# Kernel tuning notes

Measured on AMD Instinct MI355X. Metric: run time of the kernel, lower is better.

## Reference

```python
import jax, jax.numpy as jnp
import numpy as np

E = 8      # num_experts
D = 512    # input feature dim
H1 = 512   # expert_hidden[0]
H2 = 256   # expert_hidden[1]
Y = 256    # y_dim
B = 8192   # batch
ALPHA = 0.2


def setup_inputs() -> dict:
    key = jax.random.key(0)
    ks = jax.random.split(key, 8)
    h = jax.random.normal(ks[0], (B, D), dtype=jnp.float32)
    gate_id = jax.random.randint(ks[1], (B,), 0, E, dtype=jnp.int64)
    # Per-expert MLP parameters, stacked over expert axis (Glorot-ish scale)
    W1 = jax.random.normal(ks[2], (E, D, H1), dtype=jnp.float32) * (1.0 / np.sqrt(D))
    b1 = jnp.zeros((E, H1), dtype=jnp.float32)
    W2 = jax.random.normal(ks[3], (E, H1, H2), dtype=jnp.float32) * (1.0 / np.sqrt(H1))
    b2 = jnp.zeros((E, H2), dtype=jnp.float32)
    W3 = jax.random.normal(ks[4], (E, H2, Y), dtype=jnp.float32) * (1.0 / np.sqrt(H2))
    b3 = jnp.zeros((E, Y), dtype=jnp.float32)
    return {"h": h, "gate_id": gate_id, "W1": W1, "b1": b1,
            "W2": W2, "b2": b2, "W3": W3, "b3": b3}


def _leaky(x):
    return jnp.where(x > 0, x, ALPHA * x)


def reference(h, gate_id, W1, b1, W2, b2, W3, b3):
    # Hard routing: gate_id = clip(round(gate_id), 0, E-1)
    g = jnp.clip(jnp.round(gate_id.astype(jnp.float32)).astype(jnp.int32), 0, E - 1)
    # Dense all-experts compute (jit-friendly, no dynamic shapes), then select
    # the routed expert's output per row. Same math as dispatch/stitch.
    a1 = _leaky(jnp.einsum('bd,edh->ebh', h, W1) + b1[:, None, :])   # [E,B,H1]
    a2 = _leaky(jnp.einsum('ebh,ehk->ebk', a1, W2) + b2[:, None, :]) # [E,B,H2]
    y = jnp.einsum('ebk,eky->eby', a2, W3) + b3[:, None, :]          # [E,B,Y]
    out = y[g, jnp.arange(h.shape[0])]                                # [B,Y]
    return out
```

## Files before the change

kernel.cpp:

```cpp
#include <hip/hip_runtime.h>
#include <stdint.h>

#define NE 8
#define ND 512
#define NH1 512
#define NH2 256
#define NY 256
#define NB 8192
#define BM3 48
#define NBPE 24
#define NBLK (NE * NBPE)
#define W1T64 (NE * (ND/64) * (NH1/64))
#define W2T64 (NE * (NH1/64) * (NH2/64))
#define W3T64 (NE * (NH2/64) * (NY/64))
#define WTT64 (W1T64 + W2T64 + W3T64)

typedef float f32x4 __attribute__((ext_vector_type(4)));
typedef __bf16 bf16x8 __attribute__((ext_vector_type(8)));
typedef unsigned short u16x8 __attribute__((ext_vector_type(8)));

__device__ __forceinline__ unsigned short f2bf(float f) {
  unsigned int u = __float_as_uint(f);
  u += 0x7fffu + ((u >> 16) & 1u);
  return (unsigned short)(u >> 16);
}

__device__ __forceinline__ int clampe(int g) {
  return g < 0 ? 0 : (g > NE - 1 ? NE - 1 : g);
}



__global__ __launch_bounds__(256)
void prep_k(const int* __restrict__ gate,
            const float* __restrict__ W1, const float* __restrict__ W2,
            const float* __restrict__ W3,
            unsigned short* __restrict__ w1f, unsigned short* __restrict__ w2f,
            unsigned short* __restrict__ w3f,
            int* __restrict__ meta, int* __restrict__ perm)
{
  __shared__ char sm[17024] __attribute__((aligned(16)));
  int b = blockIdx.x, t = threadIdx.x;

  if (b < WTT64) {
    float* ldsf = (float*)sm;
    const float* src; unsigned short* dst; int K, N, idx;
    if (b < W1T64)          { src = W1; dst = w1f; K = ND;  N = NH1; idx = b; }
    else if (b < W1T64 + W2T64) { src = W2; dst = w2f; K = NH1; N = NH2; idx = b - W1T64; }
    else                    { src = W3; dst = w3f; K = NH2; N = NY;  idx = b - W1T64 - W2T64; }
    int ntn = N >> 6, ntk = K >> 6;
    int n0 = (idx % ntn) * 64;
    int k0 = ((idx / ntn) % ntk) * 64;
    int g  = idx / (ntn * ntk);

    {
      int r  = t >> 2;
      int c4 = t & 3;
      const float* s = src + (size_t)g * K * N + (size_t)(k0 + r) * N + n0;
      #pragma unroll
      for (int i = 0; i < 4; i++) {
        float4 v = *(const float4*)(s + (i * 4 + c4) * 4);
        *(float4*)(ldsf + r * 65 + (i * 4 + c4) * 4) = v;
      }
    }
    __syncthreads();

    unsigned short* d = dst + (size_t)g * K * N;
    #pragma unroll
    for (int ii = 0; ii < 2; ii++) {
      int idx2 = ii * 256 + t;
      int lane = idx2 & 63;
      int f    = (idx2 >> 6) & 3;
      int kt   = idx2 >> 8;
      int kl   = kt * 32 + (lane >> 4) * 8;
      int nl   = f * 16 + (lane & 15);
      union { u16x8 v; unsigned short u[8]; } pk;
      #pragma unroll
      for (int j = 0; j < 8; j++)
        pk.u[j] = f2bf(ldsf[(kl + j) * 65 + nl]);
      int ktg = (k0 >> 5) + kt;
      int fg  = (n0 >> 4) + f;
      *(u16x8*)(d + (((size_t)ktg * (N >> 4) + fg) * 64 + lane) * 8) = pk.v;
    }
    return;
  }

  unsigned int* lcnt_lo = (unsigned int*)sm;
  unsigned int* lcnt_hi = lcnt_lo + 256;
  int* pre   = (int*)(sm + 2048);
  int* cnt8  = (int*)(sm + 2048 + 8192);
  int* offs8 = cnt8 + 8;

  unsigned int gp[8];
  unsigned int clo = 0, chi = 0;
  #pragma unroll
  for (int i = 0; i < 32; i++) {
    int g = clampe(gate[t * 32 + i]);
    if ((i & 3) == 0) gp[i >> 2] = 0;
    gp[i >> 2] |= (unsigned int)g << (8 * (i & 3));
    if (g < 4) clo += 1u << (8 * g);
    else       chi += 1u << (8 * (g - 4));
  }
  lcnt_lo[t] = clo;
  lcnt_hi[t] = chi;
  __syncthreads();

  int wave = t >> 6, lane = t & 63;
  #pragma unroll
  for (int pass = 0; pass < 2; pass++) {
    int e = wave + pass * 4;
    int carry = 0;
    #pragma unroll
    for (int ch = 0; ch < 4; ch++) {
      int idx = ch * 64 + lane;
      unsigned int word = (e < 4) ? lcnt_lo[idx] : lcnt_hi[idx];
      int v = (int)((word >> (8 * (e & 3))) & 255u);
      int s = v;
      #pragma unroll
      for (int d = 1; d < 64; d <<= 1) {
        int up = __shfl_up(s, d, 64);
        if (lane >= d) s += up;
      }
      pre[e * 256 + idx] = carry + s - v;
      carry += __shfl(s, 63, 64);
    }
    if (lane == 0) cnt8[e] = carry;
  }
  __syncthreads();

  if (t == 0) {
    int off = 0;
    for (int e = 0; e < NE; e++) {
      int cc = cnt8[e];
      meta[e] = cc;
      meta[8 + e] = off;
      offs8[e] = off;
      meta[16 + e] = (cc + BM3 - 1) / BM3;
      meta[32 + e] = 0;
      off += cc;
    }
  }
  __syncthreads();

  unsigned int rlo = 0, rhi = 0;
  #pragma unroll
  for (int i = 0; i < 32; i++) {
    int g = (int)((gp[i >> 2] >> (8 * (i & 3))) & 255u);
    int r;
    if (g < 4) { r = (int)((rlo >> (8 * g)) & 255u);       rlo += 1u << (8 * g); }
    else       { r = (int)((rhi >> (8 * (g - 4))) & 255u); rhi += 1u << (8 * (g - 4)); }
    perm[offs8[g] + pre[g * 256 + t] + r] = t * 32 + i;
  }
}

__global__ __launch_bounds__(512, 4)
void mlp_k(const float* __restrict__ h,
           const float* __restrict__ b1, const float* __restrict__ b2,
           const float* __restrict__ b3,
           float* __restrict__ out,
           int* __restrict__ meta, const int* __restrict__ perm,
           const unsigned short* __restrict__ w1f,
           const unsigned short* __restrict__ w2f,
           const unsigned short* __restrict__ w3f)
{
  __shared__ unsigned short sA[BM3 * 520];
  __shared__ unsigned short sB[BM3 * 520];
  __shared__ int permc[BM3];
  __shared__ int sclaim[2];

  int tid  = threadIdx.x;

  if (tid == 0) {
    int xcc = (int)__builtin_amdgcn_s_getreg((31 << 11) | 20) & (NE - 1);
    int ce = -1, cti = 0;
    for (int a = 0; a < NE; a++) {
      int ee = (xcc + a) & (NE - 1);
      int ntl = meta[16 + ee];
      if (ntl <= 0) continue;
      int tk = atomicAdd(&meta[32 + ee], 1);
      if (tk < ntl) { ce = ee; cti = tk; break; }
    }
    sclaim[0] = ce; sclaim[1] = cti;
  }
  __syncthreads();

  int e = sclaim[0];
  if (e < 0) return;
  int trow = sclaim[1];
  int cnt  = meta[e];
  int off  = meta[8 + e];
  int row0 = trow * BM3;

  if (tid < BM3) {
    int grow = row0 + tid;
    permc[tid] = (grow < cnt) ? perm[off + grow] : 0;
  }
  __syncthreads();

  int wave = tid >> 6, lane = tid & 63;
  int lm = lane & 15, quad = lane >> 4;

  {
    int rr0 = tid >> 4;
    int cb  = (tid & 15) * 8;
    for (int r = rr0; r < BM3; r += 32) {
      const float* hrow = h + (size_t)permc[r] * ND;
      #pragma unroll
      for (int jj = 0; jj < 4; jj++) {
        int col = cb + jj * 128;
        float4 f0 = *(const float4*)(hrow + col);
        float4 f1 = *(const float4*)(hrow + col + 4);
        union { u16x8 v; unsigned short u[8]; } pk;
        pk.u[0] = f2bf(f0.x); pk.u[1] = f2bf(f0.y); pk.u[2] = f2bf(f0.z); pk.u[3] = f2bf(f0.w);
        pk.u[4] = f2bf(f1.x); pk.u[5] = f2bf(f1.y); pk.u[6] = f2bf(f1.z); pk.u[7] = f2bf(f1.w);
        *(u16x8*)(sA + r * 520 + col) = pk.v;
      }
    }
  }
  __syncthreads();

  f32x4 zero = {0.f, 0.f, 0.f, 0.f};

  {
    f32x4 acc[3][4];
    #pragma unroll
    for (int mi = 0; mi < 3; mi++)
      #pragma unroll
      for (int ni = 0; ni < 4; ni++)
        acc[mi][ni] = zero;
    const unsigned short* Wb = w1f + (size_t)e * ND * NH1 + ((size_t)(wave * 4) * 64 + lane) * 8;
    bf16x8 cur[4], nxt[4];
    #pragma unroll
    for (int ni = 0; ni < 4; ni++)
      cur[ni] = *reinterpret_cast<const bf16x8*>(Wb + ni * 512);
    for (int t = 0; t < 16; t++) {
      int tn = (t + 1 < 16) ? t + 1 : t;
      #pragma unroll
      for (int ni = 0; ni < 4; ni++)
        nxt[ni] = *reinterpret_cast<const bf16x8*>(Wb + (size_t)tn * 16384 + ni * 512);
      bf16x8 af[3];
      #pragma unroll
      for (int mi = 0; mi < 3; mi++)
        af[mi] = *reinterpret_cast<const bf16x8*>(sA + (mi * 16 + lm) * 520 + t * 32 + quad * 8);
      #pragma unroll
      for (int mi = 0; mi < 3; mi++)
        #pragma unroll
        for (int ni = 0; ni < 4; ni++)
          acc[mi][ni] = __builtin_amdgcn_mfma_f32_16x16x32_bf16(af[mi], cur[ni], acc[mi][ni], 0, 0, 0);
      #pragma unroll
      for (int ni = 0; ni < 4; ni++)
        cur[ni] = nxt[ni];
    }
    #pragma unroll
    for (int mi = 0; mi < 3; mi++)
      #pragma unroll
      for (int ni = 0; ni < 4; ni++) {
        int col = (wave * 4 + ni) * 16 + lm;
        float bv = b1[e * NH1 + col];
        #pragma unroll
        for (int r = 0; r < 4; r++) {
          int row = mi * 16 + quad * 4 + r;
          float v = acc[mi][ni][r] + bv;
          v = (v > 0.f) ? v : 0.2f * v;
          sB[row * 520 + col] = f2bf(v);
        }
      }
  }
  __syncthreads();

  {
    f32x4 acc[3][2];
    #pragma unroll
    for (int mi = 0; mi < 3; mi++)
      #pragma unroll
      for (int ni = 0; ni < 2; ni++)
        acc[mi][ni] = zero;
    const unsigned short* Wb = w2f + (size_t)e * NH1 * NH2 + ((size_t)(wave * 2) * 64 + lane) * 8;
    bf16x8 cur[2], nxt[2];
    #pragma unroll
    for (int ni = 0; ni < 2; ni++)
      cur[ni] = *reinterpret_cast<const bf16x8*>(Wb + ni * 512);
    for (int t = 0; t < 16; t++) {
      int tn = (t + 1 < 16) ? t + 1 : t;
      #pragma unroll
      for (int ni = 0; ni < 2; ni++)
        nxt[ni] = *reinterpret_cast<const bf16x8*>(Wb + (size_t)tn * 8192 + ni * 512);
      bf16x8 af[3];
      #pragma unroll
      for (int mi = 0; mi < 3; mi++)
        af[mi] = *reinterpret_cast<const bf16x8*>(sB + (mi * 16 + lm) * 520 + t * 32 + quad * 8);
      #pragma unroll
      for (int mi = 0; mi < 3; mi++)
        #pragma unroll
        for (int ni = 0; ni < 2; ni++)
          acc[mi][ni] = __builtin_amdgcn_mfma_f32_16x16x32_bf16(af[mi], cur[ni], acc[mi][ni], 0, 0, 0);
      #pragma unroll
      for (int ni = 0; ni < 2; ni++)
        cur[ni] = nxt[ni];
    }
    #pragma unroll
    for (int mi = 0; mi < 3; mi++)
      #pragma unroll
      for (int ni = 0; ni < 2; ni++) {
        int col = (wave * 2 + ni) * 16 + lm;
        float bv = b2[e * NH2 + col];
        #pragma unroll
        for (int r = 0; r < 4; r++) {
          int row = mi * 16 + quad * 4 + r;
          float v = acc[mi][ni][r] + bv;
          v = (v > 0.f) ? v : 0.2f * v;
          sA[row * 264 + col] = f2bf(v);
        }
      }
  }
  __syncthreads();

  {
    f32x4 acc[3][2];
    #pragma unroll
    for (int mi = 0; mi < 3; mi++)
      #pragma unroll
      for (int ni = 0; ni < 2; ni++)
        acc[mi][ni] = zero;
    const unsigned short* Wb = w3f + (size_t)e * NH2 * NY + ((size_t)(wave * 2) * 64 + lane) * 8;
    bf16x8 cur[2], nxt[2];
    #pragma unroll
    for (int ni = 0; ni < 2; ni++)
      cur[ni] = *reinterpret_cast<const bf16x8*>(Wb + ni * 512);
    for (int t = 0; t < 8; t++) {
      int tn = (t + 1 < 8) ? t + 1 : t;
      #pragma unroll
      for (int ni = 0; ni < 2; ni++)
        nxt[ni] = *reinterpret_cast<const bf16x8*>(Wb + (size_t)tn * 8192 + ni * 512);
      bf16x8 af[3];
      #pragma unroll
      for (int mi = 0; mi < 3; mi++)
        af[mi] = *reinterpret_cast<const bf16x8*>(sA + (mi * 16 + lm) * 264 + t * 32 + quad * 8);
      #pragma unroll
      for (int mi = 0; mi < 3; mi++)
        #pragma unroll
        for (int ni = 0; ni < 2; ni++)
          acc[mi][ni] = __builtin_amdgcn_mfma_f32_16x16x32_bf16(af[mi], cur[ni], acc[mi][ni], 0, 0, 0);
      #pragma unroll
      for (int ni = 0; ni < 2; ni++)
        cur[ni] = nxt[ni];
    }
    #pragma unroll
    for (int mi = 0; mi < 3; mi++)
      #pragma unroll
      for (int ni = 0; ni < 2; ni++) {
        int col = (wave * 2 + ni) * 16 + lm;
        float bv = b3[e * NY + col];
        #pragma unroll
        for (int r = 0; r < 4; r++) {
          int row = mi * 16 + quad * 4 + r;
          int grow = row0 + row;
          if (grow < cnt) {
            float v = acc[mi][ni][r] + bv;
            __builtin_nontemporal_store(v, &out[(size_t)permc[row] * NY + col]);
          }
        }
      }
  }
}

extern "C" void kernel_launch(void* const* d_in, const int* in_sizes, int n_in,
                              void* d_out, int out_size, void* d_ws, size_t ws_size,
                              hipStream_t stream) {
  (void)in_sizes; (void)n_in; (void)out_size; (void)ws_size;
  const float* h  = (const float*)d_in[0];
  const int* gate = (const int*)d_in[1];
  const float* W1 = (const float*)d_in[2];
  const float* b1 = (const float*)d_in[3];
  const float* W2 = (const float*)d_in[4];
  const float* b2 = (const float*)d_in[5];
  const float* W3 = (const float*)d_in[6];
  const float* b3 = (const float*)d_in[7];
  float* out = (float*)d_out;

  char* ws = (char*)d_ws;
  int* meta = (int*)ws;
  int* perm = (int*)(ws + 8192);
  unsigned short* w1f = (unsigned short*)(ws + 8192 + 32768);
  unsigned short* w2f = w1f + (size_t)NE * ND * NH1;
  unsigned short* w3f = w2f + (size_t)NE * NH1 * NH2;

  prep_k<<<WTT64 + 1, 256, 0, stream>>>(gate, W1, W2, W3, w1f, w2f, w3f, meta, perm);
  mlp_k<<<NBLK, 512, 0, stream>>>(h, b1, b2, b3, out, meta, perm, w1f, w2f, w3f);
}
```

Baseline: 113.8 us.

## Fuse weight prep and routed MLP into one cooperative kernel with grid sync

Merges the bf16 weight-conversion/routing-prep kernel and the expert MLP kernel into a single cooperative launch. Blocks first loop over the prep work units, then hit a grid-wide barrier, then compute their tile assignment statically from per-expert tile counts instead of claiming tiles with atomics. This removes one kernel launch and its inter-kernel gap. In exchange it adds grid-sync cost, the limits of a cooperative launch, and weaker XCC locality than the old atomic claim.

```diff
diff --git a/kernel.cpp b/kernel.cpp
--- a/kernel.cpp
+++ b/kernel.cpp
@@ -1,5 +1,8 @@
 #include <hip/hip_runtime.h>
+#include <hip/hip_cooperative_groups.h>
 #include <stdint.h>
+
+namespace cg = cooperative_groups;
 
 #define NE 8
 #define ND 512
@@ -8,12 +11,12 @@
 #define NY 256
 #define NB 8192
 #define BM3 48
-#define NBPE 24
-#define NBLK (NE * NBPE)
+#define NBLK 192
 #define W1T64 (NE * (ND/64) * (NH1/64))
 #define W2T64 (NE * (NH1/64) * (NH2/64))
 #define W3T64 (NE * (NH2/64) * (NY/64))
 #define WTT64 (W1T64 + W2T64 + W3T64)
+#define NUNIT (WTT64 + 1)
 
 typedef float f32x4 __attribute__((ext_vector_type(4)));
 typedef __bf16 bf16x8 __attribute__((ext_vector_type(8)));
@@ -30,163 +33,154 @@
 }
 
 
-
-__global__ __launch_bounds__(256)
-void prep_k(const int* __restrict__ gate,
-            const float* __restrict__ W1, const float* __restrict__ W2,
-            const float* __restrict__ W3,
-            unsigned short* __restrict__ w1f, unsigned short* __restrict__ w2f,
-            unsigned short* __restrict__ w3f,
-            int* __restrict__ meta, int* __restrict__ perm)
-{
-  __shared__ char sm[17024] __attribute__((aligned(16)));
-  int b = blockIdx.x, t = threadIdx.x;
-
-  if (b < WTT64) {
-    float* ldsf = (float*)sm;
-    const float* src; unsigned short* dst; int K, N, idx;
-    if (b < W1T64)          { src = W1; dst = w1f; K = ND;  N = NH1; idx = b; }
-    else if (b < W1T64 + W2T64) { src = W2; dst = w2f; K = NH1; N = NH2; idx = b - W1T64; }
-    else                    { src = W3; dst = w3f; K = NH2; N = NY;  idx = b - W1T64 - W2T64; }
-    int ntn = N >> 6, ntk = K >> 6;
-    int n0 = (idx % ntn) * 64;
-    int k0 = ((idx / ntn) % ntk) * 64;
-    int g  = idx / (ntn * ntk);
-
-    {
-      int r  = t >> 2;
-      int c4 = t & 3;
-      const float* s = src + (size_t)g * K * N + (size_t)(k0 + r) * N + n0;
-      #pragma unroll
-      for (int i = 0; i < 4; i++) {
-        float4 v = *(const float4*)(s + (i * 4 + c4) * 4);
-        *(float4*)(ldsf + r * 65 + (i * 4 + c4) * 4) = v;
-      }
-    }
-    __syncthreads();
-
-    unsigned short* d = dst + (size_t)g * K * N;
-    #pragma unroll
-    for (int ii = 0; ii < 2; ii++) {
-      int idx2 = ii * 256 + t;
-      int lane = idx2 & 63;
-      int f    = (idx2 >> 6) & 3;
-      int kt   = idx2 >> 8;
-      int kl   = kt * 32 + (lane >> 4) * 8;
-      int nl   = f * 16 + (lane & 15);
-      union { u16x8 v; unsigned short u[8]; } pk;
-      #pragma unroll
-      for (int j = 0; j < 8; j++)
-        pk.u[j] = f2bf(ldsf[(kl + j) * 65 + nl]);
-      int ktg = (k0 >> 5) + kt;
-      int fg  = (n0 >> 4) + f;
-      *(u16x8*)(d + (((size_t)ktg * (N >> 4) + fg) * 64 + lane) * 8) = pk.v;
-    }
-    return;
-  }
-
-  unsigned int* lcnt_lo = (unsigned int*)sm;
-  unsigned int* lcnt_hi = lcnt_lo + 256;
-  int* pre   = (int*)(sm + 2048);
-  int* cnt8  = (int*)(sm + 2048 + 8192);
-  int* offs8 = cnt8 + 8;
-
-  unsigned int gp[8];
-  unsigned int clo = 0, chi = 0;
-  #pragma unroll
-  for (int i = 0; i < 32; i++) {
-    int g = clampe(gate[t * 32 + i]);
-    if ((i & 3) == 0) gp[i >> 2] = 0;
-    gp[i >> 2] |= (unsigned int)g << (8 * (i & 3));
-    if (g < 4) clo += 1u << (8 * g);
-    else       chi += 1u << (8 * (g - 4));
-  }
-  lcnt_lo[t] = clo;
-  lcnt_hi[t] = chi;
-  __syncthreads();
-
-  int wave = t >> 6, lane = t & 63;
-  #pragma unroll
-  for (int pass = 0; pass < 2; pass++) {
-    int e = wave + pass * 4;
-    int carry = 0;
-    #pragma unroll
-    for (int ch = 0; ch < 4; ch++) {
-      int idx = ch * 64 + lane;
-      unsigned int word = (e < 4) ? lcnt_lo[idx] : lcnt_hi[idx];
-      int v = (int)((word >> (8 * (e & 3))) & 255u);
-      int s = v;
-      #pragma unroll
-      for (int d = 1; d < 64; d <<= 1) {
-        int up = __shfl_up(s, d, 64);
-        if (lane >= d) s += up;
-      }
-      pre[e * 256 + idx] = carry + s - v;
-      carry += __shfl(s, 63, 64);
-    }
-    if (lane == 0) cnt8[e] = carry;
-  }
-  __syncthreads();
-
-  if (t == 0) {
-    int off = 0;
-    for (int e = 0; e < NE; e++) {
-      int cc = cnt8[e];
-      meta[e] = cc;
-      meta[8 + e] = off;
-      offs8[e] = off;
-      meta[16 + e] = (cc + BM3 - 1) / BM3;
-      meta[32 + e] = 0;
-      off += cc;
-    }
-  }
-  __syncthreads();
-
-  unsigned int rlo = 0, rhi = 0;
-  #pragma unroll
-  for (int i = 0; i < 32; i++) {
-    int g = (int)((gp[i >> 2] >> (8 * (i & 3))) & 255u);
-    int r;
-    if (g < 4) { r = (int)((rlo >> (8 * g)) & 255u);       rlo += 1u << (8 * g); }
-    else       { r = (int)((rhi >> (8 * (g - 4))) & 255u); rhi += 1u << (8 * (g - 4)); }
-    perm[offs8[g] + pre[g * 256 + t] + r] = t * 32 + i;
-  }
-}
-
 __global__ __launch_bounds__(512, 4)
-void mlp_k(const float* __restrict__ h,
+void moe_k(const float* __restrict__ h, const int* __restrict__ gate,
+           const float* __restrict__ W1, const float* __restrict__ W2,
+           const float* __restrict__ W3,
            const float* __restrict__ b1, const float* __restrict__ b2,
            const float* __restrict__ b3,
            float* __restrict__ out,
-           int* __restrict__ meta, const int* __restrict__ perm,
-           const unsigned short* __restrict__ w1f,
-           const unsigned short* __restrict__ w2f,
-           const unsigned short* __restrict__ w3f)
+           int* __restrict__ meta, int* __restrict__ perm,
+           unsigned short* __restrict__ w1f, unsigned short* __restrict__ w2f,
+           unsigned short* __restrict__ w3f)
 {
-  __shared__ unsigned short sA[BM3 * 520];
-  __shared__ unsigned short sB[BM3 * 520];
-  __shared__ int permc[BM3];
-  __shared__ int sclaim[2];
-
-  int tid  = threadIdx.x;
-
-  if (tid == 0) {
-    int xcc = (int)__builtin_amdgcn_s_getreg((31 << 11) | 20) & (NE - 1);
-    int ce = -1, cti = 0;
-    for (int a = 0; a < NE; a++) {
-      int ee = (xcc + a) & (NE - 1);
+  __shared__ char smem[100032] __attribute__((aligned(16)));
+  unsigned short* sA = (unsigned short*)smem;
+  unsigned short* sB = sA + BM3 * 520;
+  int* permc = (int*)(smem + 99840);
+
+  int bid = blockIdx.x, tid = threadIdx.x;
+
+  for (int ui = 0; ui < 5; ui++) {
+    int u = bid + ui * NBLK;
+    if (u >= NUNIT) break;
+
+    if (u < WTT64) {
+      float* ldsf = (float*)smem;
+      const float* src; unsigned short* dst; int K, N, idx;
+      if (u < W1T64)              { src = W1; dst = w1f; K = ND;  N = NH1; idx = u; }
+      else if (u < W1T64 + W2T64) { src = W2; dst = w2f; K = NH1; N = NH2; idx = u - W1T64; }
+      else                        { src = W3; dst = w3f; K = NH2; N = NY;  idx = u - W1T64 - W2T64; }
+      int ntn = N >> 6, ntk = K >> 6;
+      int n0 = (idx % ntn) * 64;
+      int k0 = ((idx / ntn) % ntk) * 64;
+      int g  = idx / (ntn * ntk);
+
+      {
+        int r  = tid >> 3;
+        int c4 = tid & 7;
+        const float* s = src + (size_t)g * K * N + (size_t)(k0 + r) * N + n0;
+        #pragma unroll
+        for (int i = 0; i < 2; i++) {
+          float4 v = *(const float4*)(s + (i * 8 + c4) * 4);
+          *(float4*)(ldsf + r * 65 + (i * 8 + c4) * 4) = v;
+        }
+      }
+      __syncthreads();
+
+      {
+        unsigned short* d = dst + (size_t)g * K * N;
+        int lane = tid & 63;
+        int f    = (tid >> 6) & 3;
+        int kt   = tid >> 8;
+        int kl   = kt * 32 + (lane >> 4) * 8;
+        int nl   = f * 16 + (lane & 15);
+        union { u16x8 v; unsigned short u[8]; } pk;
+        #pragma unroll
+        for (int j = 0; j < 8; j++)
+          pk.u[j] = f2bf(ldsf[(kl + j) * 65 + nl]);
+        int ktg = (k0 >> 5) + kt;
+        int fg  = (n0 >> 4) + f;
+        *(u16x8*)(d + (((size_t)ktg * (N >> 4) + fg) * 64 + lane) * 8) = pk.v;
+      }
+    } else {
+      unsigned int* lcnt_lo = (unsigned int*)smem;
+      unsigned int* lcnt_hi = lcnt_lo + 256;
+      int* pre   = (int*)(smem + 2048);
+      int* cnt8  = (int*)(smem + 2048 + 8192);
+      int* offs8 = cnt8 + 8;
+
+      unsigned int gp[8];
+      if (tid < 256) {
+        unsigned int clo = 0, chi = 0;
+        #pragma unroll
+        for (int i = 0; i < 32; i++) {
+          int g = clampe(gate[tid * 32 + i]);
+          if ((i & 3) == 0) gp[i >> 2] = 0;
+          gp[i >> 2] |= (unsigned int)g << (8 * (i & 3));
+          if (g < 4) clo += 1u << (8 * g);
+          else       chi += 1u << (8 * (g - 4));
+        }
+        lcnt_lo[tid] = clo;
+        lcnt_hi[tid] = chi;
+      }
+      __syncthreads();
+
+      {
+        int wave = tid >> 6, lane = tid & 63;
+        int e = wave;
+        int carry = 0;
+        #pragma unroll
+        for (int ch = 0; ch < 4; ch++) {
+          int idx = ch * 64 + lane;
+          unsigned int word = (e < 4) ? lcnt_lo[idx] : lcnt_hi[idx];
+          int v = (int)((word >> (8 * (e & 3))) & 255u);
+          int s = v;
+          #pragma unroll
+          for (int d = 1; d < 64; d <<= 1) {
+            int up = __shfl_up(s, d, 64);
+            if (lane >= d) s += up;
+          }
+          pre[e * 256 + idx] = carry + s - v;
+          carry += __shfl(s, 63, 64);
+        }
+        if (lane == 0) cnt8[e] = carry;
+      }
+      __syncthreads();
+
+      if (tid == 0) {
+        int off = 0;
+        for (int e = 0; e < NE; e++) {
+          int cc = cnt8[e];
+          meta[e] = cc;
+          meta[8 + e] = off;
+          offs8[e] = off;
+          meta[16 + e] = (cc + BM3 - 1) / BM3;
+          off += cc;
+        }
+      }
+      __syncthreads();
+
+      if (tid < 256) {
+        unsigned int rlo = 0, rhi = 0;
+        #pragma unroll
+        for (int i = 0; i < 32; i++) {
+          int g = (int)((gp[i >> 2] >> (8 * (i & 3))) & 255u);
+          int r;
+          if (g < 4) { r = (int)((rlo >> (8 * g)) & 255u);       rlo += 1u << (8 * g); }
+          else       { r = (int)((rhi >> (8 * (g - 4))) & 255u); rhi += 1u << (8 * (g - 4)); }
+          perm[offs8[g] + pre[g * 256 + tid] + r] = tid * 32 + i;
+        }
+      }
+    }
+    __syncthreads();
+  }
+
+  __threadfence();
+  cg::this_grid().sync();
+
+  int e = -1, trow = 0;
+  {
+    int acc = 0;
+    #pragma unroll
+    for (int ee = 0; ee < NE; ee++) {
       int ntl = meta[16 + ee];
-      if (ntl <= 0) continue;
-      int tk = atomicAdd(&meta[32 + ee], 1);
-      if (tk < ntl) { ce = ee; cti = tk; break; }
-    }
-    sclaim[0] = ce; sclaim[1] = cti;
-  }
-  __syncthreads();
-
-  int e = sclaim[0];
+      if (e < 0 && bid < acc + ntl) { e = ee; trow = bid - acc; }
+      acc += ntl;
+    }
+  }
   if (e < 0) return;
-  int trow = sclaim[1];
+
   int cnt  = meta[e];
   int off  = meta[8 + e];
   int row0 = trow * BM3;
@@ -385,6 +379,11 @@
   unsigned short* w2f = w1f + (size_t)NE * ND * NH1;
   unsigned short* w3f = w2f + (size_t)NE * NH1 * NH2;
 
-  prep_k<<<WTT64 + 1, 256, 0, stream>>>(gate, W1, W2, W3, w1f, w2f, w3f, meta, perm);
-  mlp_k<<<NBLK, 512, 0, stream>>>(h, b1, b2, b3, out, meta, perm, w1f, w2f, w3f);
+  void* args[] = {
+    (void*)&h, (void*)&gate, (void*)&W1, (void*)&W2, (void*)&W3,
+    (void*)&b1, (void*)&b2, (void*)&b3, (void*)&out,
+    (void*)&meta, (void*)&perm, (void*)&w1f, (void*)&w2f, (void*)&w3f
+  };
+  hipLaunchCooperativeKernel((const void*)moe_k, dim3(NBLK), dim3(512),
+                             args, 0, stream);
 }
```

Result: slower. 194.5 us (+70.9%).
